# Performance work log

Hardware: AMD Instinct MI355X
Metric: run time of the kernel (lower is better)

## Reference

```python
import jax, jax.numpy as jnp
import numpy as np

N_NODES = 100000


def gcn_layer(x, src, dst, W, b, n_nodes):
    # GCNConv (PyG semantics): h = x @ W; add self-loops; symmetric norm;
    # out[dst] += norm_e * h[src]; out += bias
    h = x @ W  # [N, out_c]
    n = n_nodes
    src_sl = jnp.concatenate([src, jnp.arange(n, dtype=src.dtype)])
    dst_sl = jnp.concatenate([dst, jnp.arange(n, dtype=dst.dtype)])
    ones = jnp.ones(src_sl.shape[0], dtype=h.dtype)
    deg = jax.ops.segment_sum(ones, dst_sl, num_segments=n)  # in-degree incl self-loop
    dis = jnp.where(deg > 0, jax.lax.rsqrt(deg), 0.0)
    norm = dis[src_sl] * dis[dst_sl]  # [E+N]
    msgs = h[src_sl] * norm[:, None]  # per-edge gather (memory-bound)
    out = jax.ops.segment_sum(msgs, dst_sl, num_segments=n)
    return out + b


def setup_inputs() -> dict:
    key = jax.random.key(0)
    ks = jax.random.split(key, 8)
    in_c, out_c = 128, 64
    h1, h2, h3 = 4 * out_c, 2 * out_c, out_c  # 256, 128, 64
    n_edges = 1_600_000
    x = jax.random.normal(ks[0], (N_NODES, in_c), dtype=jnp.float32)
    edge_index = jax.random.randint(ks[1], (2, n_edges), 0, N_NODES, dtype=jnp.int64)
    def glorot(k, fan_in, fan_out):
        lim = jnp.sqrt(6.0 / (fan_in + fan_out)).astype(jnp.float32)
        return jax.random.uniform(k, (fan_in, fan_out), jnp.float32, -lim, lim)
    return {
        "x": x,
        "edge_index": edge_index,
        "W1": glorot(ks[2], in_c, h1), "b1": jnp.zeros((h1,), jnp.float32),
        "W2": glorot(ks[3], h1, h2), "b2": jnp.zeros((h2,), jnp.float32),
        "W3": glorot(ks[4], h2, h3), "b3": jnp.zeros((h3,), jnp.float32),
    }


def reference(x, edge_index, W1, b1, W2, b2, W3, b3):
    src, dst = edge_index[0], edge_index[1]
    n = x.shape[0]
    h = jax.nn.relu(gcn_layer(x, src, dst, W1, b1, n))
    h = jax.nn.relu(gcn_layer(h, src, dst, W2, b2, n))
    return gcn_layer(h, src, dst, W3, b3, n)
```

## Files before the change

kernel.cpp:

```cpp
#include <hip/hip_runtime.h>
#include <hip/hip_fp16.h>

static inline int cdiv(long long a, long long b) { return (int)((a + b - 1) / b); }

typedef _Float16 half8 __attribute__((ext_vector_type(8)));
typedef float f32x4 __attribute__((ext_vector_type(4)));

#define NBSH 8
#define BCAP 6144
#define BCHUNK 8192

__global__ void k_zero_bin(int* bcnt, int* ovf_cnt, int nbk) {
    int t = blockIdx.x * blockDim.x + threadIdx.x;
    if (t < nbk) bcnt[t] = 0;
    if (t == 0) *ovf_cnt = 0;
}

__global__ __launch_bounds__(256) void k_bin(const int* __restrict__ ei, int E, int nbk,
                                             int* __restrict__ bcnt,
                                             int2* __restrict__ ebuf,
                                             int2* __restrict__ ovf, int* __restrict__ ovf_cnt) {
    __shared__ int hist[1024];
    __shared__ int base[1024];
    const int tid = threadIdx.x;
    const int e0 = blockIdx.x * BCHUNK;
    if (e0 >= E) return;
    const int n = min(BCHUNK, E - e0);
    const int* __restrict__ srcs = ei + e0;
    const int* __restrict__ dsts = ei + E + e0;

    for (int i = tid; i < nbk; i += 256) hist[i] = 0;
    __syncthreads();
    for (int i = tid; i < n; i += 256) atomicAdd(&hist[dsts[i] >> NBSH], 1);
    __syncthreads();
    for (int b = tid; b < nbk; b += 256) {
        int h = hist[b];
        base[b] = h ? atomicAdd(&bcnt[b], h) : 0;
        hist[b] = 0;
    }
    __syncthreads();
    for (int i = tid; i < n; i += 256) {
        int d = dsts[i];
        int s = srcs[i];
        int b = d >> NBSH;
        int pos = base[b] + atomicAdd(&hist[b], 1);
        if (pos < BCAP) {
            ebuf[(size_t)b * BCAP + pos] = make_int2(s, d);
        } else {
            int op = atomicAdd(ovf_cnt, 1);
            ovf[op] = make_int2(s, d);
        }
    }
}

__global__ __launch_bounds__(1024) void k_bscan(const int* __restrict__ bcnt,
                                                int* __restrict__ bbase,
                                                int* __restrict__ row_ptr, int nbk, int N) {
    __shared__ int s[1024];
    const int t = threadIdx.x;
    int v = (t < nbk) ? bcnt[t] : 0;
    s[t] = v;
    __syncthreads();
    for (int off = 1; off < 1024; off <<= 1) {
        int u = (t >= off) ? s[t - off] : 0;
        __syncthreads();
        s[t] += u;
        __syncthreads();
    }
    if (t < nbk) bbase[t] = s[t] - v;
    if (t == nbk - 1) row_ptr[N] = s[t];
}

__global__ __launch_bounds__(256) void k_passB1(const int* __restrict__ bcnt,
                                                const int* __restrict__ bbase,
                                                const int2* __restrict__ ebuf,
                                                const int2* __restrict__ ovf,
                                                const int* __restrict__ ovf_cnt,
                                                int* __restrict__ row_ptr,
                                                float* __restrict__ dis, int N) {
    __shared__ int ldeg[256];
    __shared__ int sc[256];
    const int tid = threadIdx.x;
    const int b = blockIdx.x;
    const int d0 = b << NBSH;
    const int dn = min(1 << NBSH, N - d0);
    ldeg[tid] = 0;
    __syncthreads();
    const int sz = min(bcnt[b], BCAP);
    const int2* __restrict__ reg = ebuf + (size_t)b * BCAP;
    for (int i = tid; i < sz; i += 256) atomicAdd(&ldeg[reg[i].y - d0], 1);
    const int oc = *ovf_cnt;
    for (int i = tid; i < oc; i += 256) {
        int d = ovf[i].y;
        if ((d >> NBSH) == b) atomicAdd(&ldeg[d - d0], 1);
    }
    __syncthreads();
    sc[tid] = ldeg[tid];
    __syncthreads();
    for (int off = 1; off < 256; off <<= 1) {
        int u = (tid >= off) ? sc[tid - off] : 0;
        __syncthreads();
        sc[tid] += u;
        __syncthreads();
    }
    if (tid < dn) {
        row_ptr[d0 + tid] = bbase[b] + sc[tid] - ldeg[tid];
        dis[d0 + tid] = rsqrtf((float)(ldeg[tid] + 1));
    }
}

__global__ __launch_bounds__(256) void k_passB2(const int* __restrict__ bcnt,
                                                const int2* __restrict__ ebuf,
                                                const int2* __restrict__ ovf,
                                                const int* __restrict__ ovf_cnt,
                                                const int* __restrict__ row_ptr,
                                                const float* __restrict__ dis,
                                                int2* __restrict__ csr, int N) {
    __shared__ int lcur[256];
    const int tid = threadIdx.x;
    const int b = blockIdx.x;
    const int d0 = b << NBSH;
    const int dn = min(1 << NBSH, N - d0);
    lcur[tid] = (tid < dn) ? row_ptr[d0 + tid] : 0;
    __syncthreads();
    const int sz = min(bcnt[b], BCAP);
    const int2* __restrict__ reg = ebuf + (size_t)b * BCAP;
    for (int i = tid; i < sz; i += 256) {
        int2 sd = reg[i];
        float w = dis[sd.x] * dis[sd.y];
        int pos = atomicAdd(&lcur[sd.y - d0], 1);
        csr[pos] = make_int2(sd.x, __float_as_int(w));
    }
    const int oc = *ovf_cnt;
    for (int i = tid; i < oc; i += 256) {
        int2 sd = ovf[i];
        if ((sd.y >> NBSH) != b) continue;
        float w = dis[sd.x] * dis[sd.y];
        int pos = atomicAdd(&lcur[sd.y - d0], 1);
        csr[pos] = make_int2(sd.x, __float_as_int(w));
    }
}

__global__ void k_zero_i(int* p, int n) {
    int t = blockIdx.x * blockDim.x + threadIdx.x;
    if (t < n) p[t] = 0;
}

__global__ void k_count(const int* __restrict__ dst, int* __restrict__ deg, int E) {
    int t = blockIdx.x * blockDim.x + threadIdx.x;
    if (t < E) atomicAdd(&deg[dst[t]], 1);
}

__global__ __launch_bounds__(1024) void k_scan1(const int* __restrict__ deg,
                                                int* __restrict__ tmp,
                                                int* __restrict__ bsum, int n) {
    __shared__ int s[1024];
    const int t = threadIdx.x;
    const int i = blockIdx.x * 1024 + t;
    int v = (i < n) ? deg[i] : 0;
    s[t] = v;
    __syncthreads();
    for (int off = 1; off < 1024; off <<= 1) {
        int u = (t >= off) ? s[t - off] : 0;
        __syncthreads();
        s[t] += u;
        __syncthreads();
    }
    if (i < n) tmp[i] = s[t];
    if (t == 1023) bsum[blockIdx.x] = s[1023];
}

__global__ __launch_bounds__(1024) void k_scan2(int* __restrict__ bsum, int nb) {
    __shared__ int s[1024];
    const int t = threadIdx.x;
    s[t] = (t < nb) ? bsum[t] : 0;
    __syncthreads();
    for (int off = 1; off < 1024; off <<= 1) {
        int u = (t >= off) ? s[t - off] : 0;
        __syncthreads();
        s[t] += u;
        __syncthreads();
    }
    if (t < nb) bsum[t] = s[t];
}

__global__ __launch_bounds__(1024) void k_scan3(const int* __restrict__ deg,
                                                const int* __restrict__ tmp,
                                                const int* __restrict__ bsum,
                                                int* __restrict__ row_ptr,
                                                float* __restrict__ dis,
                                                int* __restrict__ cur, int n, int nb) {
    const int i = blockIdx.x * 1024 + threadIdx.x;
    if (i < n) {
        int off = (blockIdx.x == 0) ? 0 : bsum[blockIdx.x - 1];
        int dgi = deg[i];
        int r = tmp[i] - dgi + off;
        row_ptr[i] = r;
        dis[i] = rsqrtf((float)(dgi + 1));
        cur[i] = r;
    } else if (i == n) {
        row_ptr[n] = bsum[nb - 1];
    }
}

__global__ void k_scatter(const int* __restrict__ ei, const float* __restrict__ dis,
                          int* __restrict__ cur, int2* __restrict__ csr, int E) {
    int e = blockIdx.x * blockDim.x + threadIdx.x;
    if (e >= E) return;
    int s = ei[e];
    int d = ei[e + E];
    float w = dis[s] * dis[d];
    int pos = atomicAdd(&cur[d], 1);
    csr[pos] = make_int2(s, __float_as_int(w));
}

__global__ __launch_bounds__(256) void k_cvt_h(const float* __restrict__ in,
                                               __half* __restrict__ out, long long n4) {
    long long t = (long long)blockIdx.x * blockDim.x + threadIdx.x;
    if (t >= n4) return;
    float4 v = *(const float4*)(in + t * 4);
    union { float2 f; __half2 h[2]; } u;
    u.h[0] = __floats2half2_rn(v.x, v.y);
    u.h[1] = __floats2half2_rn(v.z, v.w);
    *(float2*)(out + t * 4) = u.f;
}

template <int K, int CN>
__global__ void k_prep_wt(const float* __restrict__ W, char* __restrict__ wt) {
    constexpr int CH = K / 8;
    int id = blockIdx.x * blockDim.x + threadIdx.x;
    if (id >= CN * CH) return;
    int n = id / CH, c = id % CH;
    half8 h;
#pragma unroll
    for (int j = 0; j < 8; ++j) h[j] = (_Float16)W[(size_t)(c * 8 + j) * CN + n];
    *(half8*)(wt + (size_t)n * (2 * K) + ((c * 16) ^ ((n & 7) << 4))) = h;
}

template <int C, bool BIAS, bool RELU, bool HOUT>
__global__ __launch_bounds__(256) void k_agg_v(const int* __restrict__ row_ptr,
                                               const int2* __restrict__ csr,
                                               const float* __restrict__ dis,
                                               const _Float16* __restrict__ in,
                                               void* __restrict__ out_,
                                               const float* __restrict__ bias, int N) {
    constexpr int LPR = C / 8;
    constexpr int RPW = 64 / LPR;
    const int wave = (int)(((long long)blockIdx.x * blockDim.x + threadIdx.x) >> 6);
    const int lane = threadIdx.x & 63;
    const int d = wave * RPW + lane / LPR;
    if (d >= N) return;
    const int c = (lane % LPR) * 8;
    const _Float16* __restrict__ inc = in + c;

    float acc[8];
    {
        half8 v = *(const half8*)(inc + (size_t)d * C);
        float dd = dis[d], ws = dd * dd;
#pragma unroll
        for (int k = 0; k < 8; ++k) acc[k] = ws * (float)v[k];
    }

    int j = row_ptr[d];
    const int hi = row_ptr[d + 1];
    for (; j + 3 < hi; j += 4) {
        int2 e0 = csr[j + 0];
        int2 e1 = csr[j + 1];
        int2 e2 = csr[j + 2];
        int2 e3 = csr[j + 3];
        half8 v0 = *(const half8*)(inc + (size_t)e0.x * C);
        half8 v1 = *(const half8*)(inc + (size_t)e1.x * C);
        half8 v2 = *(const half8*)(inc + (size_t)e2.x * C);
        half8 v3 = *(const half8*)(inc + (size_t)e3.x * C);
        float w0 = __int_as_float(e0.y), w1 = __int_as_float(e1.y);
        float w2 = __int_as_float(e2.y), w3 = __int_as_float(e3.y);
#pragma unroll
        for (int k = 0; k < 8; ++k)
            acc[k] += w0 * (float)v0[k] + w1 * (float)v1[k] + w2 * (float)v2[k] + w3 * (float)v3[k];
    }
    for (; j < hi; ++j) {
        int2 e0 = csr[j];
        half8 v0 = *(const half8*)(inc + (size_t)e0.x * C);
        float w0 = __int_as_float(e0.y);
#pragma unroll
        for (int k = 0; k < 8; ++k) acc[k] += w0 * (float)v0[k];
    }

    if (BIAS) {
        float4 b0 = *(const float4*)(bias + c);
        float4 b1 = *(const float4*)(bias + c + 4);
        acc[0] += b0.x; acc[1] += b0.y; acc[2] += b0.z; acc[3] += b0.w;
        acc[4] += b1.x; acc[5] += b1.y; acc[6] += b1.z; acc[7] += b1.w;
    }
    if (RELU) {
#pragma unroll
        for (int k = 0; k < 8; ++k) acc[k] = fmaxf(acc[k], 0.f);
    }
    if constexpr (HOUT) {
        half8 h;
#pragma unroll
        for (int k = 0; k < 8; ++k) h[k] = (_Float16)acc[k];
        *(half8*)((_Float16*)out_ + (size_t)d * C + c) = h;
    } else {
        float* o = (float*)out_ + (size_t)d * C + c;
        *(float4*)o = make_float4(acc[0], acc[1], acc[2], acc[3]);
        *(float4*)(o + 4) = make_float4(acc[4], acc[5], acc[6], acc[7]);
    }
}

template <int K, int CN, bool BIAS, bool RELU>
__global__ __launch_bounds__(256) void k_gemm_mfma(const _Float16* __restrict__ A,
                                                   const char* __restrict__ wt,
                                                   const float* __restrict__ bias,
                                                   _Float16* __restrict__ C, int M) {
    constexpr int T = K / 32;
    constexpr int NT = CN / 16;
    __shared__ __align__(16) char wlds[CN * K * 2];
    const int tid = threadIdx.x;
    for (int i = tid; i < CN * K / 8; i += 256)
        ((float4*)wlds)[i] = ((const float4*)wt)[i];
    __syncthreads();

    const int l = tid & 63;
    const int w = tid >> 6;
    const int r0 = blockIdx.x * 128 + w * 32;
    const int lm = l & 15;
    const int lg = l >> 4;
    const int sw = (l & 7) << 4;

    half8 af[2][T];
#pragma unroll
    for (int s = 0; s < 2; ++s) {
        int row = r0 + s * 16 + lm;
        row = row < M ? row : M - 1;
        const _Float16* ap = A + (size_t)row * K + lg * 8;
#pragma unroll
        for (int t = 0; t < T; ++t) af[s][t] = *(const half8*)(ap + t * 32);
    }

    f32x4 acc[2][NT] = {};
#pragma unroll
    for (int j = 0; j < NT; ++j) {
        const int n = j * 16 + lm;
        const char* bp = wlds + n * (2 * K);
        half8 bf[T];
#pragma unroll
        for (int t = 0; t < T; ++t)
            bf[t] = *(const half8*)(bp + ((t * 64 + lg * 16) ^ sw));
#pragma unroll
        for (int s = 0; s < 2; ++s)
#pragma unroll
            for (int t = 0; t < T; ++t)
                acc[s][j] = __builtin_amdgcn_mfma_f32_16x16x32_f16(bf[t], af[s][t], acc[s][j], 0, 0, 0);
    }

#pragma unroll
    for (int s = 0; s < 2; ++s) {
        const int m = r0 + s * 16 + lm;
        if (m >= M) continue;
#pragma unroll
        for (int j = 0; j < NT; ++j) {
            const int n0 = j * 16 + lg * 4;
            f32x4 v = acc[s][j];
            if (BIAS) {
                float4 b = *(const float4*)(bias + n0);
                v[0] += b.x; v[1] += b.y; v[2] += b.z; v[3] += b.w;
            }
            if (RELU) {
                v[0] = fmaxf(v[0], 0.f); v[1] = fmaxf(v[1], 0.f);
                v[2] = fmaxf(v[2], 0.f); v[3] = fmaxf(v[3], 0.f);
            }
            union { float2 f; __half2 h[2]; } u;
            u.h[0] = __floats2half2_rn(v[0], v[1]);
            u.h[1] = __floats2half2_rn(v[2], v[3]);
            *(float2*)(C + (size_t)m * CN + n0) = u.f;
        }
    }
}

extern "C" void kernel_launch(void* const* d_in, const int* in_sizes, int n_in,
                              void* d_out, int out_size, void* d_ws, size_t ws_size,
                              hipStream_t stream) {
    const float* x  = (const float*)d_in[0];
    const int* ei   = (const int*)d_in[1];
    const float* W1 = (const float*)d_in[2];
    const float* b1 = (const float*)d_in[3];
    const float* W2 = (const float*)d_in[4];
    const float* b2 = (const float*)d_in[5];
    const float* W3 = (const float*)d_in[6];
    const float* b3 = (const float*)d_in[7];
    float* out = (float*)d_out;

    const int N = in_sizes[0] / 128;
    const int E = in_sizes[1] / 2;
    const int* dst = ei + E;
    const int nbk = cdiv(N, 1 << NBSH);

    char* base = (char*)d_ws;
    size_t off = 0;
    auto take = [&](size_t bytes) {
        char* r = base + off;
        off += (bytes + 255) & ~(size_t)255;
        return r;
    };
    float* dis    = (float*)take((size_t)N * 4);
    int* row_ptr  = (int*)take((size_t)(N + 1) * 4);
    int* bcnt     = (int*)take((size_t)nbk * 4);
    int* bbase    = (int*)take((size_t)nbk * 4);
    int* ovf_cnt  = (int*)take(256);
    int2* csr     = (int2*)take((size_t)E * 8);
    char* binmem  = take((size_t)nbk * BCAP * 8);
    int2* ovf     = (int2*)take((size_t)E * 8);
    _Float16* xh  = (_Float16*)take((size_t)N * 128 * 2);
    _Float16* a1  = (_Float16*)take((size_t)N * 128 * 2);
    _Float16* h1  = (_Float16*)take((size_t)N * 256 * 2);
    char* wt1     = take(256 * 128 * 2);
    char* wt2     = take(128 * 256 * 2);
    char* wt3     = take(64 * 128 * 2);
    _Float16* t2 = a1;
    _Float16* h2 = h1;
    _Float16* t3 = xh;

    const bool BUCKET = (off <= ws_size) && (nbk <= 1024);

    if (BUCKET) {
        int2* ebuf = (int2*)binmem;
        k_zero_bin<<<cdiv(nbk + 1, 256), 256, 0, stream>>>(bcnt, ovf_cnt, nbk);
        k_bin<<<cdiv(E, BCHUNK), 256, 0, stream>>>(ei, E, nbk, bcnt, ebuf, ovf, ovf_cnt);
        k_bscan<<<1, 1024, 0, stream>>>(bcnt, bbase, row_ptr, nbk, N);
        k_passB1<<<nbk, 256, 0, stream>>>(bcnt, bbase, ebuf, ovf, ovf_cnt, row_ptr, dis, N);
        k_passB2<<<nbk, 256, 0, stream>>>(bcnt, ebuf, ovf, ovf_cnt, row_ptr, dis, csr, N);
    } else {
        size_t o2 = 0;
        auto take2 = [&](size_t bytes) {
            char* r = binmem + o2;
            o2 += (bytes + 255) & ~(size_t)255;
            return r;
        };
        int* deg  = (int*)take2((size_t)N * 4);
        int* tmp  = (int*)take2((size_t)N * 4);
        int* bsum = (int*)take2((size_t)1024 * 4);
        int* cur  = (int*)take2((size_t)N * 4);
        const int nb = cdiv(N, 1024);
        k_zero_i<<<cdiv(N, 256), 256, 0, stream>>>(deg, N);
        k_count<<<cdiv(E, 256), 256, 0, stream>>>(dst, deg, E);
        k_scan1<<<nb, 1024, 0, stream>>>(deg, tmp, bsum, N);
        k_scan2<<<1, 1024, 0, stream>>>(bsum, nb);
        k_scan3<<<cdiv(N + 1, 1024), 1024, 0, stream>>>(deg, tmp, bsum, row_ptr, dis, cur, N, nb);
        k_scatter<<<cdiv(E, 256), 256, 0, stream>>>(ei, dis, cur, csr, E);
    }

    k_cvt_h<<<cdiv((long long)N * 32, 256), 256, 0, stream>>>(x, (__half*)xh, (long long)N * 32);
    k_prep_wt<128, 256><<<cdiv(256 * 16, 256), 256, 0, stream>>>(W1, wt1);
    k_prep_wt<256, 128><<<cdiv(128 * 32, 256), 256, 0, stream>>>(W2, wt2);
    k_prep_wt<128, 64><<<cdiv(64 * 16, 256), 256, 0, stream>>>(W3, wt3);

    const int gA128 = cdiv((long long)cdiv(N, 4) * 64, 256);
    const int gA64  = cdiv((long long)cdiv(N, 8) * 64, 256);
    const int gG = cdiv(N, 128);

    k_agg_v<128, false, false, true><<<gA128, 256, 0, stream>>>(row_ptr, csr, dis, xh, a1, nullptr, N);
    k_gemm_mfma<128, 256, true, true><<<gG, 256, 0, stream>>>(a1, wt1, b1, h1, N);

    k_gemm_mfma<256, 128, false, false><<<gG, 256, 0, stream>>>(h1, wt2, nullptr, t2, N);
    k_agg_v<128, true, true, true><<<gA128, 256, 0, stream>>>(row_ptr, csr, dis, t2, h2, b2, N);

    k_gemm_mfma<128, 64, false, false><<<gG, 256, 0, stream>>>(h2, wt3, nullptr, t3, N);
    k_agg_v<64, true, false, false><<<gA64, 256, 0, stream>>>(row_ptr, csr, dis, t3, out, b3, N);
}
```

Baseline: 318.2 us.

## Pack edges, merge CSR passes, drop stored weights, and degree-sort aggregation rows

Edges in the bins are packed into one int (source shifted left, local destination in the low bits), and the two per-bucket passes are merged into one kernel that stages the bucket in shared memory. The CSR now holds only the source index, so each aggregation computes the edge weight from dis on the fly, roughly halving CSR traffic. A degree histogram, scan and permutation kernel order the aggregation rows by degree so that rows handled by the same wave do similar amounts of work. The cost is three extra small kernels, an extra dis gather per edge, and less locality in destination writes. Packing source<<8 assumes source ids below 2^23.

```diff
diff --git a/kernel.cpp b/kernel.cpp
--- a/kernel.cpp
+++ b/kernel.cpp
@@ -10,15 +10,16 @@
 #define BCAP 6144
 #define BCHUNK 8192
 
-__global__ void k_zero_bin(int* bcnt, int* ovf_cnt, int nbk) {
+__global__ void k_zero_misc(int* bcnt, int nbk, int* gdh, int* ovf_cnt) {
     int t = blockIdx.x * blockDim.x + threadIdx.x;
     if (t < nbk) bcnt[t] = 0;
+    if (t < 256) gdh[t] = 0;
     if (t == 0) *ovf_cnt = 0;
 }
 
 __global__ __launch_bounds__(256) void k_bin(const int* __restrict__ ei, int E, int nbk,
                                              int* __restrict__ bcnt,
-                                             int2* __restrict__ ebuf,
+                                             int* __restrict__ ebuf,
                                              int2* __restrict__ ovf, int* __restrict__ ovf_cnt) {
     __shared__ int hist[1024];
     __shared__ int base[1024];
@@ -45,7 +46,7 @@
         int b = d >> NBSH;
         int pos = base[b] + atomicAdd(&hist[b], 1);
         if (pos < BCAP) {
-            ebuf[(size_t)b * BCAP + pos] = make_int2(s, d);
+            ebuf[(size_t)b * BCAP + pos] = (s << NBSH) | (d & ((1 << NBSH) - 1));
         } else {
             int op = atomicAdd(ovf_cnt, 1);
             ovf[op] = make_int2(s, d);
@@ -71,74 +72,115 @@
     if (t == nbk - 1) row_ptr[N] = s[t];
 }
 
-__global__ __launch_bounds__(256) void k_passB1(const int* __restrict__ bcnt,
-                                                const int* __restrict__ bbase,
-                                                const int2* __restrict__ ebuf,
-                                                const int2* __restrict__ ovf,
-                                                const int* __restrict__ ovf_cnt,
-                                                int* __restrict__ row_ptr,
-                                                float* __restrict__ dis, int N) {
+__global__ __launch_bounds__(256) void k_passB(const int* __restrict__ bcnt,
+                                               const int* __restrict__ bbase,
+                                               const int* __restrict__ ebuf,
+                                               const int2* __restrict__ ovf,
+                                               const int* __restrict__ ovf_cnt,
+                                               int* __restrict__ row_ptr,
+                                               float* __restrict__ dis,
+                                               int* __restrict__ csr, int N) {
+    __shared__ int sedge[BCAP];
     __shared__ int ldeg[256];
-    __shared__ int sc[256];
+    __shared__ int lcur[256];
     const int tid = threadIdx.x;
     const int b = blockIdx.x;
     const int d0 = b << NBSH;
-    const int dn = min(1 << NBSH, N - d0);
+    const int dn = min(256, N - d0);
     ldeg[tid] = 0;
     __syncthreads();
     const int sz = min(bcnt[b], BCAP);
-    const int2* __restrict__ reg = ebuf + (size_t)b * BCAP;
-    for (int i = tid; i < sz; i += 256) atomicAdd(&ldeg[reg[i].y - d0], 1);
+    const int* __restrict__ reg = ebuf + (size_t)b * BCAP;
+    for (int i = tid; i < sz; i += 256) {
+        int e = reg[i];
+        sedge[i] = e;
+        atomicAdd(&ldeg[e & 255], 1);
+    }
     const int oc = *ovf_cnt;
     for (int i = tid; i < oc; i += 256) {
         int d = ovf[i].y;
         if ((d >> NBSH) == b) atomicAdd(&ldeg[d - d0], 1);
     }
     __syncthreads();
-    sc[tid] = ldeg[tid];
+    const int v = ldeg[tid];
+    lcur[tid] = v;
     __syncthreads();
     for (int off = 1; off < 256; off <<= 1) {
-        int u = (tid >= off) ? sc[tid - off] : 0;
-        __syncthreads();
-        sc[tid] += u;
-        __syncthreads();
-    }
+        int u = (tid >= off) ? lcur[tid - off] : 0;
+        __syncthreads();
+        lcur[tid] += u;
+        __syncthreads();
+    }
+    const int rp = bbase[b] + lcur[tid] - v;
     if (tid < dn) {
-        row_ptr[d0 + tid] = bbase[b] + sc[tid] - ldeg[tid];
-        dis[d0 + tid] = rsqrtf((float)(ldeg[tid] + 1));
-    }
-}
-
-__global__ __launch_bounds__(256) void k_passB2(const int* __restrict__ bcnt,
-                                                const int2* __restrict__ ebuf,
-                                                const int2* __restrict__ ovf,
-                                                const int* __restrict__ ovf_cnt,
-                                                const int* __restrict__ row_ptr,
-                                                const float* __restrict__ dis,
-                                                int2* __restrict__ csr, int N) {
-    __shared__ int lcur[256];
-    const int tid = threadIdx.x;
-    const int b = blockIdx.x;
-    const int d0 = b << NBSH;
-    const int dn = min(1 << NBSH, N - d0);
-    lcur[tid] = (tid < dn) ? row_ptr[d0 + tid] : 0;
-    __syncthreads();
-    const int sz = min(bcnt[b], BCAP);
-    const int2* __restrict__ reg = ebuf + (size_t)b * BCAP;
+        row_ptr[d0 + tid] = rp;
+        dis[d0 + tid] = rsqrtf((float)(v + 1));
+    }
+    lcur[tid] = rp;
+    __syncthreads();
     for (int i = tid; i < sz; i += 256) {
-        int2 sd = reg[i];
-        float w = dis[sd.x] * dis[sd.y];
-        int pos = atomicAdd(&lcur[sd.y - d0], 1);
-        csr[pos] = make_int2(sd.x, __float_as_int(w));
-    }
-    const int oc = *ovf_cnt;
+        int e = sedge[i];
+        int pos = atomicAdd(&lcur[e & 255], 1);
+        csr[pos] = e >> NBSH;
+    }
     for (int i = tid; i < oc; i += 256) {
         int2 sd = ovf[i];
         if ((sd.y >> NBSH) != b) continue;
-        float w = dis[sd.x] * dis[sd.y];
         int pos = atomicAdd(&lcur[sd.y - d0], 1);
-        csr[pos] = make_int2(sd.x, __float_as_int(w));
-    }
+        csr[pos] = sd.x;
+    }
+}
+
+__global__ __launch_bounds__(256) void k_dhist(const int* __restrict__ row_ptr,
+                                               int* __restrict__ gdh, int N) {
+    __shared__ int h[256];
+    const int tid = threadIdx.x;
+    h[tid] = 0;
+    __syncthreads();
+    int i = blockIdx.x * 256 + tid;
+    if (i < N) {
+        int deg = min(row_ptr[i + 1] - row_ptr[i], 255);
+        atomicAdd(&h[deg], 1);
+    }
+    __syncthreads();
+    if (h[tid]) atomicAdd(&gdh[tid], h[tid]);
+}
+
+__global__ __launch_bounds__(256) void k_dscan(const int* __restrict__ gdh,
+                                               int* __restrict__ dbase) {
+    __shared__ int s[256];
+    const int t = threadIdx.x;
+    int v = gdh[t];
+    s[t] = v;
+    __syncthreads();
+    for (int off = 1; off < 256; off <<= 1) {
+        int u = (t >= off) ? s[t - off] : 0;
+        __syncthreads();
+        s[t] += u;
+        __syncthreads();
+    }
+    dbase[t] = s[t] - v;
+}
+
+__global__ __launch_bounds__(256) void k_dperm(const int* __restrict__ row_ptr,
+                                               int* __restrict__ dbase,
+                                               int* __restrict__ perm, int N) {
+    __shared__ int h[256];
+    __shared__ int base[256];
+    const int tid = threadIdx.x;
+    const int i = blockIdx.x * 256 + tid;
+    h[tid] = 0;
+    __syncthreads();
+    int deg = -1, lr = 0;
+    if (i < N) {
+        deg = min(row_ptr[i + 1] - row_ptr[i], 255);
+        lr = atomicAdd(&h[deg], 1);
+    }
+    __syncthreads();
+    int c = h[tid];
+    base[tid] = c ? atomicAdd(&dbase[tid], c) : 0;
+    __syncthreads();
+    if (i < N) perm[base[deg] + lr] = i;
 }
 
 __global__ void k_zero_i(int* p, int n) {
@@ -203,15 +245,14 @@
     }
 }
 
-__global__ void k_scatter(const int* __restrict__ ei, const float* __restrict__ dis,
-                          int* __restrict__ cur, int2* __restrict__ csr, int E) {
+__global__ void k_scatter(const int* __restrict__ ei,
+                          int* __restrict__ cur, int* __restrict__ csr, int E) {
     int e = blockIdx.x * blockDim.x + threadIdx.x;
     if (e >= E) return;
     int s = ei[e];
     int d = ei[e + E];
-    float w = dis[s] * dis[d];
     int pos = atomicAdd(&cur[d], 1);
-    csr[pos] = make_int2(s, __float_as_int(w));
+    csr[pos] = s;
 }
 
 __global__ __launch_bounds__(256) void k_cvt_h(const float* __restrict__ in,
@@ -239,7 +280,8 @@
 
 template <int C, bool BIAS, bool RELU, bool HOUT>
 __global__ __launch_bounds__(256) void k_agg_v(const int* __restrict__ row_ptr,
-                                               const int2* __restrict__ csr,
+                                               const int* __restrict__ csr,
+                                               const int* __restrict__ perm,
                                                const float* __restrict__ dis,
                                                const _Float16* __restrict__ in,
                                                void* __restrict__ out_,
@@ -248,15 +290,17 @@
     constexpr int RPW = 64 / LPR;
     const int wave = (int)(((long long)blockIdx.x * blockDim.x + threadIdx.x) >> 6);
     const int lane = threadIdx.x & 63;
-    const int d = wave * RPW + lane / LPR;
-    if (d >= N) return;
+    const int r = wave * RPW + lane / LPR;
+    if (r >= N) return;
+    const int d = perm[r];
     const int c = (lane % LPR) * 8;
     const _Float16* __restrict__ inc = in + c;
+    const float ddis = dis[d];
 
     float acc[8];
     {
         half8 v = *(const half8*)(inc + (size_t)d * C);
-        float dd = dis[d], ws = dd * dd;
+        float ws = ddis * ddis;
 #pragma unroll
         for (int k = 0; k < 8; ++k) acc[k] = ws * (float)v[k];
     }
@@ -264,24 +308,24 @@
     int j = row_ptr[d];
     const int hi = row_ptr[d + 1];
     for (; j + 3 < hi; j += 4) {
-        int2 e0 = csr[j + 0];
-        int2 e1 = csr[j + 1];
-        int2 e2 = csr[j + 2];
-        int2 e3 = csr[j + 3];
-        half8 v0 = *(const half8*)(inc + (size_t)e0.x * C);
-        half8 v1 = *(const half8*)(inc + (size_t)e1.x * C);
-        half8 v2 = *(const half8*)(inc + (size_t)e2.x * C);
-        half8 v3 = *(const half8*)(inc + (size_t)e3.x * C);
-        float w0 = __int_as_float(e0.y), w1 = __int_as_float(e1.y);
-        float w2 = __int_as_float(e2.y), w3 = __int_as_float(e3.y);
+        int s0 = csr[j + 0];
+        int s1 = csr[j + 1];
+        int s2 = csr[j + 2];
+        int s3 = csr[j + 3];
+        half8 v0 = *(const half8*)(inc + (size_t)s0 * C);
+        half8 v1 = *(const half8*)(inc + (size_t)s1 * C);
+        half8 v2 = *(const half8*)(inc + (size_t)s2 * C);
+        half8 v3 = *(const half8*)(inc + (size_t)s3 * C);
+        float w0 = dis[s0] * ddis, w1 = dis[s1] * ddis;
+        float w2 = dis[s2] * ddis, w3 = dis[s3] * ddis;
 #pragma unroll
         for (int k = 0; k < 8; ++k)
             acc[k] += w0 * (float)v0[k] + w1 * (float)v1[k] + w2 * (float)v2[k] + w3 * (float)v3[k];
     }
     for (; j < hi; ++j) {
-        int2 e0 = csr[j];
-        half8 v0 = *(const half8*)(inc + (size_t)e0.x * C);
-        float w0 = __int_as_float(e0.y);
+        int s0 = csr[j];
+        half8 v0 = *(const half8*)(inc + (size_t)s0 * C);
+        float w0 = dis[s0] * ddis;
 #pragma unroll
         for (int k = 0; k < 8; ++k) acc[k] += w0 * (float)v0[k];
     }
@@ -405,11 +449,14 @@
     };
     float* dis    = (float*)take((size_t)N * 4);
     int* row_ptr  = (int*)take((size_t)(N + 1) * 4);
+    int* perm     = (int*)take((size_t)N * 4);
     int* bcnt     = (int*)take((size_t)nbk * 4);
     int* bbase    = (int*)take((size_t)nbk * 4);
+    int* gdh      = (int*)take(256 * 4);
+    int* dbase    = (int*)take(256 * 4);
     int* ovf_cnt  = (int*)take(256);
-    int2* csr     = (int2*)take((size_t)E * 8);
-    char* binmem  = take((size_t)nbk * BCAP * 8);
+    int* csr      = (int*)take((size_t)E * 4);
+    char* binmem  = take((size_t)nbk * BCAP * 4);
     int2* ovf     = (int2*)take((size_t)E * 8);
     _Float16* xh  = (_Float16*)take((size_t)N * 128 * 2);
     _Float16* a1  = (_Float16*)take((size_t)N * 128 * 2);
@@ -423,13 +470,13 @@
 
     const bool BUCKET = (off <= ws_size) && (nbk <= 1024);
 
+    k_zero_misc<<<cdiv(nbk > 256 ? nbk : 256, 256), 256, 0, stream>>>(bcnt, nbk, gdh, ovf_cnt);
+
     if (BUCKET) {
-        int2* ebuf = (int2*)binmem;
-        k_zero_bin<<<cdiv(nbk + 1, 256), 256, 0, stream>>>(bcnt, ovf_cnt, nbk);
+        int* ebuf = (int*)binmem;
         k_bin<<<cdiv(E, BCHUNK), 256, 0, stream>>>(ei, E, nbk, bcnt, ebuf, ovf, ovf_cnt);
         k_bscan<<<1, 1024, 0, stream>>>(bcnt, bbase, row_ptr, nbk, N);
-        k_passB1<<<nbk, 256, 0, stream>>>(bcnt, bbase, ebuf, ovf, ovf_cnt, row_ptr, dis, N);
-        k_passB2<<<nbk, 256, 0, stream>>>(bcnt, ebuf, ovf, ovf_cnt, row_ptr, dis, csr, N);
+        k_passB<<<nbk, 256, 0, stream>>>(bcnt, bbase, ebuf, ovf, ovf_cnt, row_ptr, dis, csr, N);
     } else {
         size_t o2 = 0;
         auto take2 = [&](size_t bytes) {
@@ -447,8 +494,12 @@
         k_scan1<<<nb, 1024, 0, stream>>>(deg, tmp, bsum, N);
         k_scan2<<<1, 1024, 0, stream>>>(bsum, nb);
         k_scan3<<<cdiv(N + 1, 1024), 1024, 0, stream>>>(deg, tmp, bsum, row_ptr, dis, cur, N, nb);
-        k_scatter<<<cdiv(E, 256), 256, 0, stream>>>(ei, dis, cur, csr, E);
-    }
+        k_scatter<<<cdiv(E, 256), 256, 0, stream>>>(ei, cur, csr, E);
+    }
+
+    k_dhist<<<cdiv(N, 256), 256, 0, stream>>>(row_ptr, gdh, N);
+    k_dscan<<<1, 256, 0, stream>>>(gdh, dbase);
+    k_dperm<<<cdiv(N, 256), 256, 0, stream>>>(row_ptr, dbase, perm, N);
 
     k_cvt_h<<<cdiv((long long)N * 32, 256), 256, 0, stream>>>(x, (__half*)xh, (long long)N * 32);
     k_prep_wt<128, 256><<<cdiv(256 * 16, 256), 256, 0, stream>>>(W1, wt1);
@@ -459,12 +510,12 @@
     const int gA64  = cdiv((long long)cdiv(N, 8) * 64, 256);
     const int gG = cdiv(N, 128);
 
-    k_agg_v<128, false, false, true><<<gA128, 256, 0, stream>>>(row_ptr, csr, dis, xh, a1, nullptr, N);
+    k_agg_v<128, false, false, true><<<gA128, 256, 0, stream>>>(row_ptr, csr, perm, dis, xh, a1, nullptr, N);
     k_gemm_mfma<128, 256, true, true><<<gG, 256, 0, stream>>>(a1, wt1, b1, h1, N);
 
     k_gemm_mfma<256, 128, false, false><<<gG, 256, 0, stream>>>(h1, wt2, nullptr, t2, N);
-    k_agg_v<128, true, true, true><<<gA128, 256, 0, stream>>>(row_ptr, csr, dis, t2, h2, b2, N);
+    k_agg_v<128, true, true, true><<<gA128, 256, 0, stream>>>(row_ptr, csr, perm, dis, t2, h2, b2, N);
 
     k_gemm_mfma<128, 64, false, false><<<gG, 256, 0, stream>>>(h2, wt3, nullptr, t3, N);
-    k_agg_v<64, true, false, false><<<gA64, 256, 0, stream>>>(row_ptr, csr, dis, t3, out, b3, N);
-}
+    k_agg_v<64, true, false, false><<<gA64, 256, 0, stream>>>(row_ptr, csr, perm, dis, t3, out, b3, N);
+}
```

After: 323.2 us. Within noise of the previous version (+1.6%).
